# Optimization experiments

Hardware: AMD Instinct MI355X
Metric: run time of the kernel (lower is better)

## Reference

```python
import jax, jax.numpy as jnp
import numpy as np

C = 256      # in_channels
H = 16       # num_heads
K = 7        # tconv kernel size
P1 = 8       # type_1 partition size
P2 = 8       # type_2 partition size
HB = H // 4  # heads per attention branch (= 4)
EPS = 1e-5


def _ln(x, g, b):
    m = x.mean(-1, keepdims=True)
    v = ((x - m) ** 2).mean(-1, keepdims=True)
    return (x - m) / jnp.sqrt(v + EPS) * g + b


def _window_attn(parts, table, heads, P):
    # parts: [B_, P, 3*Cb]; table: [2P-1, heads]
    B_, N, _ = parts.shape
    qkv = parts.reshape(B_, N, 3, heads, -1).transpose(2, 0, 3, 1, 4)  # [3,B_,h,P,d]
    q, k, v = qkv[0], qkv[1], qkv[2]
    scale = heads ** (-0.5)  # NOTE: module scales by num_heads**-0.5 (faithful)
    attn = jnp.einsum('bhnd,bhmd->bhnm', q * scale, k)
    idx = (jnp.arange(P)[:, None] - jnp.arange(P)[None, :]) + P - 1  # [P,P]
    bias = table[idx].transpose(2, 0, 1)  # [h,P,P]
    attn = jax.nn.softmax(attn + bias[None], axis=-1)
    out = jnp.einsum('bhnm,bhmd->bhnd', attn, v)
    return out.transpose(0, 2, 1, 3).reshape(B_, N, -1)


def _type1_part(x, P):  # x: [B,Cc,T] contiguous windows
    B, Cc, T = x.shape
    return x.reshape(B, Cc, T // P, P).transpose(0, 2, 3, 1).reshape(-1, P, Cc)


def _type1_rev(y, B, Cc, T, P):
    return y.reshape(B, T // P, P, Cc).transpose(0, 3, 1, 2).reshape(B, Cc, T)


def _type2_part(x, P):  # strided (dilated) windows
    B, Cc, T = x.shape
    return x.reshape(B, Cc, P, T // P).transpose(0, 3, 2, 1).reshape(-1, P, Cc)


def _type2_rev(y, B, Cc, T, P):
    return y.reshape(B, T // P, P, Cc).transpose(0, 3, 2, 1).reshape(B, Cc, T)


def setup_inputs() -> dict:
    key = jax.random.key(0)
    ks = jax.random.split(key, 16)
    B, T = 16, 8192
    d = {
        'x': jax.random.normal(ks[0], (B, C, T), jnp.float32),
        'g1': jnp.ones((C,), jnp.float32),
        'b1': jnp.zeros((C,), jnp.float32),
        'Wm': jax.random.normal(ks[1], (C, 2 * C), jnp.float32) * 0.02,
        'bm': jnp.zeros((2 * C,), jnp.float32),
        'Wc': jax.random.normal(ks[2], (C // 2, (C // 2) // (H // 2), K), jnp.float32) * 0.05,
        'bc': jnp.zeros((C // 2,), jnp.float32),
        'tab1': jax.random.normal(ks[3], (2 * P1 - 1, HB), jnp.float32) * 0.02,
        'tab2': jax.random.normal(ks[4], (2 * P2 - 1, HB), jnp.float32) * 0.02,
        'Wp': jax.random.normal(ks[5], (C, C), jnp.float32) * 0.02,
        'bp': jnp.zeros((C,), jnp.float32),
        'g2': jnp.ones((C,), jnp.float32),
        'b2': jnp.zeros((C,), jnp.float32),
        'W1': jax.random.normal(ks[6], (C, 4 * C), jnp.float32) * 0.02,
        'bf1': jnp.zeros((4 * C,), jnp.float32),
        'W2': jax.random.normal(ks[7], (4 * C, C), jnp.float32) * 0.02,
        'bf2': jnp.zeros((C,), jnp.float32),
    }
    return d


def _forward(x, g1, b1, Wm, bm, Wc, bc, tab1, tab2, Wp, bp, g2, b2, W1, bf1, W2, bf2):
    B, Cin, T = x.shape
    xt = x.transpose(0, 2, 1)  # [B,T,C]
    skip = xt
    f = (_ln(xt, g1, b1) @ Wm + bm).transpose(0, 2, 1)  # [B,2C,T]
    f_conv, f_attn = f[:, :Cin // 2], f[:, Cin // 2:]
    # grouped temporal conv, padding SAME
    y0 = jax.lax.conv_general_dilated(
        f_conv, Wc, window_strides=(1,), padding=[((K - 1) // 2, (K - 1) // 2)],
        feature_group_count=H // 2, dimension_numbers=('NCH', 'OIH', 'NCH')) + bc[None, :, None]
    Cb3 = 3 * Cin // 4
    fa1, fa2 = f_attn[:, :Cb3], f_attn[:, Cb3:]
    y1 = _type1_rev(_window_attn(_type1_part(fa1, P1), tab1, HB, P1), B, Cin // 4, T, P1)
    y2 = _type2_rev(_window_attn(_type2_part(fa2, P2), tab2, HB, P2), B, Cin // 4, T, P2)
    out = jnp.concatenate([y0, y1, y2], axis=1).transpose(0, 2, 1) @ Wp + bp
    out = skip + out
    h = _ln(out, g2, b2)
    h = jax.nn.gelu(h @ W1 + bf1, approximate=False) @ W2 + bf2
    out = out + h
    return out.transpose(0, 2, 1)  # [B,C,T]


def reference(x, g1, b1, Wm, bm, Wc, bc, tab1, tab2, Wp, bp, g2, b2, W1, bf1, W2, bf2):
    return _forward(x, g1, b1, Wm, bm, Wc, bc, tab1, tab2, Wp, bp, g2, b2, W1, bf1, W2, bf2)
```

## Files before the change

kernel.cpp:

```cpp
#include <hip/hip_runtime.h>
#include <hip/hip_bf16.h>

#define DI __device__ __forceinline__

typedef unsigned short u16;
typedef __attribute__((ext_vector_type(4))) float f32x4;
typedef __attribute__((ext_vector_type(8))) short short8;
typedef __attribute__((ext_vector_type(4))) short short4v;

constexpr int Bb = 16, Tt = 8192;
constexpr int M_TOT = Bb * Tt;

static DI u16 f2bf(float f) {
    union { float f; unsigned u; } v; v.f = f;
    unsigned r = v.u + 0x7fffu + ((v.u >> 16) & 1u);
    return (u16)(r >> 16);
}
static DI float bf2f(u16 u) {
    union { unsigned u; float f; } v; v.u = ((unsigned)u) << 16;
    return v.f;
}
static DI float bf2f_s(short s) { return bf2f((u16)s); }

static DI void lds_load16(const void* g, void* l) {
    __builtin_amdgcn_global_load_lds(
        (const __attribute__((address_space(1))) void*)g,
        (__attribute__((address_space(3))) void*)l, 16, 0, 0);
}

static DI float gelu_exact(float x) {
    float ax = fabsf(x) * 0.70710678118654752f;
    float t = __builtin_amdgcn_rcpf(1.f + 0.3275911f * ax);
    float y = t * (0.254829592f + t * (-0.284496736f + t * (1.421413741f +
              t * (-1.453152027f + t * 1.061405429f))));
    float e = __expf(-ax * ax);
    float erf = 1.f - y * e;
    erf = copysignf(erf, x);
    return 0.5f * x * (1.f + erf);
}

__global__ void prep_weights(const float* __restrict__ Wm, const float* __restrict__ Wp,
                             const float* __restrict__ W1, const float* __restrict__ W2,
                             const float* __restrict__ Wc,
                             u16* __restrict__ WmT, u16* __restrict__ WpT,
                             u16* __restrict__ W1T, u16* __restrict__ W2T,
                             u16* __restrict__ WtC) {
    int i = blockIdx.x * blockDim.x + threadIdx.x;
    int stride = gridDim.x * blockDim.x;
    for (int j = i; j < 512 * 256; j += stride) {
        int n = j >> 8, k = j & 255;
        WmT[j] = f2bf(Wm[k * 512 + n]);
    }
    for (int j = i; j < 256 * 256; j += stride) {
        int n = j >> 8, k = j & 255;
        WpT[j] = f2bf(Wp[k * 256 + n]);
    }
    for (int j = i; j < 1024 * 256; j += stride) {
        int n = j >> 8, k = j & 255;
        W1T[j] = f2bf(W1[k * 1024 + n]);
    }
    for (int j = i; j < 256 * 1024; j += stride) {
        int n = j >> 10, k = j & 1023;
        W2T[j] = f2bf(W2[k * 256 + n]);
    }
    for (int j = i; j < 128 * 128; j += stride) {
        int co = j >> 7, kp = j & 127;
        int tap = kp >> 4, ci = kp & 15;
        float v = (tap < 7) ? Wc[(co * 16 + ci) * 7 + tap] : 0.f;
        WtC[j] = f2bf(v);
    }
}

__global__ __launch_bounds__(256) void ln1_kernel(const float* __restrict__ x,
                                                  const float* __restrict__ g1,
                                                  const float* __restrict__ b1,
                                                  u16* __restrict__ xln,
                                                  u16* __restrict__ xt) {
    __shared__ u16 tile[64 * 256];
    __shared__ float ps[64 * 16], pss[64 * 16];
    __shared__ float smean[64], srstd[64];
    int bidx = blockIdx.x;
    int b = bidx >> 7;
    int t0 = (bidx & 127) << 6;
    int tid = threadIdx.x, l = tid & 63, w = tid >> 6;
    int lr = l & 15, lg = l >> 4;
    float s[4] = {}, ss[4] = {};
    #pragma unroll 4
    for (int it = 0; it < 16; ++it) {
        int c = it * 16 + w * 4 + lg;
        f32x4 v = *(const f32x4*)&x[((size_t)b * 256 + c) * 8192 + t0 + lr * 4];
        #pragma unroll
        for (int k = 0; k < 4; ++k) {
            s[k] += v[k]; ss[k] += v[k] * v[k];
            int t = lr * 4 + k;
            int c8 = c >> 3;
            int slot = (c8 & 24) | ((c8 ^ t) & 7);
            tile[t * 256 + slot * 8 + (c & 7)] = f2bf(v[k]);
        }
    }
    #pragma unroll
    for (int k = 0; k < 4; ++k) {
        ps[(lr * 4 + k) * 16 + w * 4 + lg] = s[k];
        pss[(lr * 4 + k) * 16 + w * 4 + lg] = ss[k];
    }
    __syncthreads();
    if (tid < 64) {
        float sum = 0.f, sq = 0.f;
        #pragma unroll
        for (int g = 0; g < 16; ++g) { sum += ps[tid * 16 + g]; sq += pss[tid * 16 + g]; }
        float m = sum * (1.f / 256.f);
        smean[tid] = m;
        srstd[tid] = rsqrtf(sq * (1.f / 256.f) - m * m + 1e-5f);
    }
    __syncthreads();
    int r = tid >> 2, q = tid & 3;
    float m = smean[r], rs = srstd[r];
    size_t rowbase = ((size_t)b * 8192 + t0 + r) * 256;
    #pragma unroll
    for (int u = 0; u < 8; ++u) {
        int c0 = q * 64 + u * 8;
        int c8 = c0 >> 3;
        int slot = (c8 & 24) | ((c8 ^ r) & 7);
        short8 d = *(const short8*)&tile[r * 256 + slot * 8];
        *(short8*)&xt[rowbase + c0] = d;
        short8 o;
        #pragma unroll
        for (int j = 0; j < 8; ++j) {
            int c = c0 + j;
            o[j] = (short)f2bf((bf2f_s(d[j]) - m) * rs * g1[c] + b1[c]);
        }
        *(short8*)&xln[rowbase + c0] = o;
    }
}

template<int EPI, int N, int K>
__global__ __launch_bounds__(256) void gemm_bt2(const u16* __restrict__ A,
                                                const u16* __restrict__ Bt,
                                                const float* __restrict__ bias,
                                                u16* __restrict__ outb,
                                                const u16* __restrict__ skipx) {
    constexpr int NB = N / 128;
    int bid = blockIdx.x;
    int x8 = bid & 7;
    int rest = bid >> 3;
    int ni = rest % NB;
    int mi = (rest / NB) * 8 + x8;
    int m0 = mi * 128, n0 = ni * 128;
    __shared__ u16 As[2][128 * 64];
    __shared__ u16 Bs[2][128 * 64];
    int tid = threadIdx.x, l = tid & 63, w = tid >> 6;
    int mrow = (w >> 1) * 64, ncol = (w & 1) * 64;
    int lr = l & 15, lg = l >> 4;
    f32x4 acc[4][4] = {};
    auto stage = [&](int buf, int k0) {
        #pragma unroll
        for (int p = 0; p < 4; ++p) {
            int cb = p * 256 + w * 64;
            int chunk = cb + l;
            int row = chunk >> 3, k8 = chunk & 7;
            int k8s = k8 ^ (row & 7);
            lds_load16(A  + (size_t)(m0 + row) * K + k0 + k8s * 8, &As[buf][cb * 8]);
            lds_load16(Bt + (size_t)(n0 + row) * K + k0 + k8s * 8, &Bs[buf][cb * 8]);
        }
    };
    stage(0, 0);
    __syncthreads();
    constexpr int NT = K / 64;
    int buf = 0;
    for (int t = 0; t < NT; ++t) {
        if (t + 1 < NT) stage(buf ^ 1, (t + 1) * 64);
        #pragma unroll
        for (int kk = 0; kk < 64; kk += 32) {
            short8 a[4], bfr[4];
            #pragma unroll
            for (int i = 0; i < 4; ++i) {
                int r = mrow + i * 16 + lr;
                a[i] = *(const short8*)&As[buf][r * 64 + ((((kk >> 3) + lg) ^ (r & 7)) << 3)];
            }
            #pragma unroll
            for (int j = 0; j < 4; ++j) {
                int r = ncol + j * 16 + lr;
                bfr[j] = *(const short8*)&Bs[buf][r * 64 + ((((kk >> 3) + lg) ^ (r & 7)) << 3)];
            }
            #pragma unroll
            for (int i = 0; i < 4; ++i)
                #pragma unroll
                for (int j = 0; j < 4; ++j)
                    acc[i][j] = __builtin_amdgcn_mfma_f32_16x16x32_bf16(a[i], bfr[j], acc[i][j], 0, 0, 0);
        }
        __syncthreads();
        buf ^= 1;
    }
    #pragma unroll
    for (int i = 0; i < 4; ++i) {
        int row0 = m0 + mrow + i * 16 + lg * 4;
        #pragma unroll
        for (int j = 0; j < 4; ++j) {
            int col = n0 + ncol + j * 16 + lr;
            float bv = bias[col];
            f32x4 v = acc[i][j];
            if constexpr (EPI == 0) {
                #pragma unroll
                for (int r = 0; r < 4; ++r)
                    outb[(size_t)(row0 + r) * N + col] = f2bf(v[r] + bv);
            } else {
                #pragma unroll
                for (int r = 0; r < 4; ++r)
                    outb[(size_t)(row0 + r) * N + col] =
                        f2bf(v[r] + bv + bf2f(skipx[(size_t)(row0 + r) * 256 + col]));
            }
        }
    }
}

__global__ __launch_bounds__(512) void ffn_fused(const u16* __restrict__ lnb,
                                                 const u16* __restrict__ W1T,
                                                 const float* __restrict__ bf1v,
                                                 const u16* __restrict__ W2T,
                                                 const float* __restrict__ bf2v,
                                                 const u16* __restrict__ outb,
                                                 float* __restrict__ out) {
    __shared__ u16 Aln[128 * 256];
    __shared__ u16 W1c[64 * 256];
    __shared__ u16 W2c[256 * 64];
    __shared__ u16 hbuf[128 * 64];
    int bid = blockIdx.x;
    int m0 = bid * 128;
    int tid = threadIdx.x, l = tid & 63, w = tid >> 6;
    int lr = l & 15, lg = l >> 4;
    int wm1 = w >> 1, wn1 = w & 1;
    int wm2 = w >> 2, wn2 = w & 3;

    #pragma unroll
    for (int p = 0; p < 8; ++p) {
        int cb = p * 512 + w * 64;
        int chunk = cb + l;
        int row = chunk >> 5, c8 = chunk & 31;
        int c8s = (c8 & 24) | ((c8 ^ row) & 7);
        lds_load16(lnb + (size_t)(m0 + row) * 256 + c8s * 8, &Aln[cb * 8]);
    }
    auto stageW1 = [&](int c) {
        #pragma unroll
        for (int p = 0; p < 4; ++p) {
            int cb = p * 512 + w * 64;
            int chunk = cb + l;
            int row = chunk >> 5, c8 = chunk & 31;
            int c8s = (c8 & 24) | ((c8 ^ row) & 7);
            lds_load16(W1T + (size_t)(c * 64 + row) * 256 + c8s * 8, &W1c[cb * 8]);
        }
    };
    auto stageW2 = [&](int c) {
        #pragma unroll
        for (int p = 0; p < 4; ++p) {
            int cb = p * 512 + w * 64;
            int chunk = cb + l;
            int row = chunk >> 3, c8 = chunk & 7;
            int c8s = (c8 ^ row) & 7;
            lds_load16(W2T + (size_t)row * 1024 + c * 64 + c8s * 8, &W2c[cb * 8]);
        }
    };
    stageW1(0);
    stageW2(0);
    f32x4 acc2[4][4] = {};
    __syncthreads();

    for (int c = 0; c < 16; ++c) {
        f32x4 acc1[2][2] = {};
        #pragma unroll
        for (int ks = 0; ks < 8; ++ks) {
            int c8 = ks * 4 + lg;
            short8 a[2], bb[2];
            #pragma unroll
            for (int i = 0; i < 2; ++i) {
                int r = wm1 * 32 + i * 16 + lr;
                a[i] = *(const short8*)&Aln[r * 256 + (((c8 & 24) | ((c8 ^ r) & 7)) << 3)];
            }
            #pragma unroll
            for (int j = 0; j < 2; ++j) {
                int n = wn1 * 32 + j * 16 + lr;
                bb[j] = *(const short8*)&W1c[n * 256 + (((c8 & 24) | ((c8 ^ n) & 7)) << 3)];
            }
            #pragma unroll
            for (int i = 0; i < 2; ++i)
                #pragma unroll
                for (int j = 0; j < 2; ++j)
                    acc1[i][j] = __builtin_amdgcn_mfma_f32_16x16x32_bf16(a[i], bb[j], acc1[i][j], 0, 0, 0);
        }
        __syncthreads();
        if (c < 15) stageW1(c + 1);
        #pragma unroll
        for (int i = 0; i < 2; ++i) {
            int row = wm1 * 32 + i * 16 + lg * 4;
            #pragma unroll
            for (int j = 0; j < 2; ++j) {
                int col = wn1 * 32 + j * 16 + lr;
                int c8h = col >> 3;
                #pragma unroll
                for (int r = 0; r < 4; ++r) {
                    float vv = gelu_exact(acc1[i][j][r] + bf1v[c * 64 + col]);
                    hbuf[(row + r) * 64 + (((c8h ^ (row + r)) & 7) << 3) + (col & 7)] = f2bf(vv);
                }
            }
        }
        __syncthreads();
        #pragma unroll
        for (int ks = 0; ks < 2; ++ks) {
            int c8 = ks * 4 + lg;
            short8 a[4], bb[4];
            #pragma unroll
            for (int i = 0; i < 4; ++i) {
                int r = wm2 * 64 + i * 16 + lr;
                a[i] = *(const short8*)&hbuf[r * 64 + (((c8 ^ (r & 7)) & 7) << 3)];
            }
            #pragma unroll
            for (int j = 0; j < 4; ++j) {
                int n = wn2 * 64 + j * 16 + lr;
                bb[j] = *(const short8*)&W2c[n * 64 + (((c8 ^ (n & 7)) & 7) << 3)];
            }
            #pragma unroll
            for (int i = 0; i < 4; ++i)
                #pragma unroll
                for (int j = 0; j < 4; ++j)
                    acc2[i][j] = __builtin_amdgcn_mfma_f32_16x16x32_bf16(a[i], bb[j], acc2[i][j], 0, 0, 0);
        }
        __syncthreads();
        if (c < 15) stageW2(c + 1);
    }
    int bidx_b = m0 >> 13;
    int tbase = m0 & 8191;
    #pragma unroll
    for (int i = 0; i < 4; ++i) {
        int row0 = wm2 * 64 + i * 16 + lg * 4;
        #pragma unroll
        for (int j = 0; j < 4; ++j) {
            int col = wn2 * 64 + j * 16 + lr;
            float bv = bf2v[col];
            f32x4 o;
            #pragma unroll
            for (int r = 0; r < 4; ++r)
                o[r] = acc2[i][j][r] + bv + bf2f(outb[(size_t)(m0 + row0 + r) * 256 + col]);
            *(f32x4*)&out[((size_t)bidx_b * 256 + col) * 8192 + tbase + row0] = o;
        }
    }
}

__global__ __launch_bounds__(256) void conv_kernel(const u16* __restrict__ f,
                                                   const u16* __restrict__ WtC,
                                                   const float* __restrict__ bc,
                                                   u16* __restrict__ att) {
    __shared__ u16 fs[72 * 128];
    __shared__ u16 wt[128 * 128];
    int bid = blockIdx.x;
    int b = bid >> 7;
    int t0 = (bid & 127) << 6;
    int tid = threadIdx.x, l = tid & 63, w = tid >> 6;
    for (int c = tid; c < 2048; c += 256) {
        int row = c >> 4, c8 = c & 15;
        int slot = (c8 & 8) | ((c8 ^ row) & 7);
        *(uint4*)&wt[row * 128 + slot * 8] = *(const uint4*)&WtC[c * 8];
    }
    for (int c = tid; c < 72 * 16; c += 256) {
        int rrow = c >> 4, c8 = c & 15;
        int t = t0 - 3 + rrow;
        uint4 v = {0u, 0u, 0u, 0u};
        if (t >= 0 && t < 8192)
            v = *(const uint4*)&f[((size_t)b * 8192 + t) * 512 + c8 * 8];
        int slot = (c8 & 8) | ((c8 ^ rrow) & 7);
        *(uint4*)&fs[rrow * 128 + slot * 8] = v;
    }
    __syncthreads();
    int wr = w >> 1, wc = w & 1;
    int lr = l & 15, lg = l >> 4;
    f32x4 acc[2][4] = {};
    #pragma unroll
    for (int kk = 0; kk < 4; ++kk) {
        int kp = kk * 32 + lg * 8;
        int tap = kp >> 4, ci = kp & 15;
        #pragma unroll
        for (int i = 0; i < 2; ++i) {
            int trow = wr * 32 + i * 16 + lr;
            #pragma unroll
            for (int g = 0; g < 4; ++g) {
                int ra = trow + tap;
                int ea = (wc * 4 + g) * 2 + (ci >> 3);
                short8 a = *(const short8*)&fs[ra * 128 + (((ea & 8) | ((ea ^ ra) & 7)) << 3)];
                int nb = (wc * 4 + g) * 16 + lr;
                int eb = kp >> 3;
                short8 bfr = *(const short8*)&wt[nb * 128 + (((eb & 8) | ((eb ^ nb) & 7)) << 3)];
                acc[i][g] = __builtin_amdgcn_mfma_f32_16x16x32_bf16(a, bfr, acc[i][g], 0, 0, 0);
            }
        }
    }
    #pragma unroll
    for (int i = 0; i < 2; ++i) {
        int trow = wr * 32 + i * 16 + lg * 4;
        #pragma unroll
        for (int g = 0; g < 4; ++g) {
            int co = (wc * 4 + g) * 16 + lr;
            float bv = bc[co];
            #pragma unroll
            for (int r = 0; r < 4; ++r) {
                int t = t0 + trow + r;
                att[((size_t)b * 8192 + t) * 256 + co] = f2bf(acc[i][g][r] + bv);
            }
        }
    }
}

template<int TYPE>
__global__ __launch_bounds__(256) void attn_kernel(const u16* __restrict__ f,
                                                   const float* __restrict__ tab,
                                                   u16* __restrict__ att) {
    __shared__ u16 qkv[64 * 200];
    __shared__ float stab[60];
    constexpr int QBASE = (TYPE == 1) ? 128 : 320;
    constexpr int OBASE = (TYPE == 1) ? 128 : 192;
    int bid = blockIdx.x;
    int b = bid >> 7;
    int j0 = (bid & 127) << 3;
    int tid = threadIdx.x;
    if (tid < 60) stab[tid] = tab[tid];
    for (int c = tid; c < 64 * 24; c += 256) {
        int ridx = c / 24, off = (c % 24) << 3;
        int wl = ridx >> 3, n = ridx & 7;
        int t = (TYPE == 1) ? ((j0 + wl) * 8 + n) : (n * 1024 + j0 + wl);
        *(uint4*)&qkv[ridx * 200 + off] = *(const uint4*)&f[((size_t)b * 8192 + t) * 512 + QBASE + off];
    }
    __syncthreads();
    int wl = tid >> 5, h = (tid >> 3) & 3, n = tid & 7;
    const u16* qr = &qkv[(wl * 8 + n) * 200 + h * 16];
    float q[16];
    {
        short8 q0 = *(const short8*)qr, q1 = *(const short8*)(qr + 8);
        #pragma unroll
        for (int d = 0; d < 8; ++d) { q[d] = bf2f_s(q0[d]); q[d + 8] = bf2f_s(q1[d]); }
    }
    float s[8];
    #pragma unroll
    for (int m = 0; m < 8; ++m) {
        const u16* kr = &qkv[(wl * 8 + m) * 200 + 64 + h * 16];
        short8 k0 = *(const short8*)kr, k1 = *(const short8*)(kr + 8);
        float a = 0.f;
        #pragma unroll
        for (int d = 0; d < 8; ++d) a += q[d] * bf2f_s(k0[d]) + q[d + 8] * bf2f_s(k1[d]);
        s[m] = 0.5f * a + stab[(n - m + 7) * 4 + h];
    }
    float mx = s[0];
    #pragma unroll
    for (int m = 1; m < 8; ++m) mx = fmaxf(mx, s[m]);
    float sum = 0.f;
    #pragma unroll
    for (int m = 0; m < 8; ++m) { s[m] = __expf(s[m] - mx); sum += s[m]; }
    float rinv = 1.f / sum;
    float o[16] = {};
    #pragma unroll
    for (int m = 0; m < 8; ++m) {
        float p = s[m] * rinv;
        const u16* vr = &qkv[(wl * 8 + m) * 200 + 128 + h * 16];
        short8 v0 = *(const short8*)vr, v1 = *(const short8*)(vr + 8);
        #pragma unroll
        for (int d = 0; d < 8; ++d) { o[d] += p * bf2f_s(v0[d]); o[d + 8] += p * bf2f_s(v1[d]); }
    }
    int t = (TYPE == 1) ? ((j0 + wl) * 8 + n) : (n * 1024 + j0 + wl);
    short8 o0, o1;
    #pragma unroll
    for (int d = 0; d < 8; ++d) { o0[d] = (short)f2bf(o[d]); o1[d] = (short)f2bf(o[d + 8]); }
    u16* op = &att[((size_t)b * 8192 + t) * 256 + OBASE + h * 16];
    *(short8*)op = o0; *(short8*)(op + 8) = o1;
}

__global__ __launch_bounds__(256) void ln2_kernel(const u16* __restrict__ outb,
                                                  const float* __restrict__ g2,
                                                  const float* __restrict__ b2,
                                                  u16* __restrict__ ln2o) {
    int row = blockIdx.x * 4 + (threadIdx.x >> 6);
    int l = threadIdx.x & 63;
    const u16* rp = &outb[(size_t)row * 256 + l * 4];
    short4v d = *(const short4v*)rp;
    float v[4];
    float sum = 0.f, ss = 0.f;
    #pragma unroll
    for (int j = 0; j < 4; ++j) {
        v[j] = bf2f_s(d[j]);
        sum += v[j]; ss += v[j] * v[j];
    }
    #pragma unroll
    for (int off = 32; off; off >>= 1) {
        sum += __shfl_xor(sum, off);
        ss  += __shfl_xor(ss, off);
    }
    float mean = sum * (1.f / 256.f);
    float var = ss * (1.f / 256.f) - mean * mean;
    float rstd = rsqrtf(var + 1e-5f);
    short4v o;
    #pragma unroll
    for (int j = 0; j < 4; ++j) {
        int c = l * 4 + j;
        o[j] = (short)f2bf((v[j] - mean) * rstd * g2[c] + b2[c]);
    }
    *(short4v*)&ln2o[(size_t)row * 256 + l * 4] = o;
}

extern "C" void kernel_launch(void* const* d_in, const int* in_sizes, int n_in,
                              void* d_out, int out_size, void* d_ws, size_t ws_size,
                              hipStream_t stream) {
    const float* x    = (const float*)d_in[0];
    const float* g1   = (const float*)d_in[1];
    const float* b1   = (const float*)d_in[2];
    const float* Wm   = (const float*)d_in[3];
    const float* bm   = (const float*)d_in[4];
    const float* Wc   = (const float*)d_in[5];
    const float* bc   = (const float*)d_in[6];
    const float* tab1 = (const float*)d_in[7];
    const float* tab2 = (const float*)d_in[8];
    const float* Wp   = (const float*)d_in[9];
    const float* bp   = (const float*)d_in[10];
    const float* g2   = (const float*)d_in[11];
    const float* b2   = (const float*)d_in[12];
    const float* W1   = (const float*)d_in[13];
    const float* bf1  = (const float*)d_in[14];
    const float* W2   = (const float*)d_in[15];
    const float* bf2  = (const float*)d_in[16];
    float* out = (float*)d_out;

    char* ws = (char*)d_ws;
    u16* f    = (u16*)(ws);
    u16* att  = (u16*)(ws + 134217728);
    u16* outb = (u16*)(ws + 201326592);
    u16* lnb  = (u16*)(ws + 268435456);
    u16* xt   = (u16*)(ws + 335544320);
    char* wb = ws + 402653184;
    u16* WmT = (u16*)wb;
    u16* WpT = (u16*)(wb + 262144);
    u16* W1T = (u16*)(wb + 393216);
    u16* W2T = (u16*)(wb + 917504);
    u16* WtC = (u16*)(wb + 1441792);

    prep_weights<<<512, 256, 0, stream>>>(Wm, Wp, W1, W2, Wc, WmT, WpT, W1T, W2T, WtC);
    ln1_kernel<<<Bb * (Tt / 64), 256, 0, stream>>>(x, g1, b1, lnb, xt);
    gemm_bt2<0, 512, 256><<<(M_TOT / 128) * 4, 256, 0, stream>>>(lnb, WmT, bm, f, nullptr);
    conv_kernel<<<Bb * (Tt / 64), 256, 0, stream>>>(f, WtC, bc, att);
    attn_kernel<1><<<Bb * 128, 256, 0, stream>>>(f, tab1, att);
    attn_kernel<2><<<Bb * 128, 256, 0, stream>>>(f, tab2, att);
    gemm_bt2<1, 256, 256><<<(M_TOT / 128) * 2, 256, 0, stream>>>(att, WpT, bp, outb, xt);
    ln2_kernel<<<M_TOT / 4, 256, 0, stream>>>(outb, g2, b2, lnb);
    ffn_fused<<<M_TOT / 128, 512, 0, stream>>>(lnb, W1T, bf1, W2T, bf2, outb, out);
}
```

Before: 575.1 us.

## Fold LayerNorm affine into weights, fuse LN2 into FFN, double-buffer FFN weights

Folds the LN1 and LN2 gamma scales into the Wm and W1 weights and their betas into precomputed biases, so the LN kernels only normalize. Removes the separate ln2 kernel by computing row statistics inside the FFN kernel from register-resident A fragments, and double-buffers the W1/W2 chunk staging to overlap loads with MFMA. Also replaces exact erf GELU with a sigmoid-style approximation and adds s_setprio around MFMA loops. The GELU approximation and the bf16 rounding of scaled weights change numerics slightly.

After: 524.5 us. 8.8% less time.

```diff
diff --git a/kernel.cpp b/kernel.cpp
--- a/kernel.cpp
+++ b/kernel.cpp
@@ -21,6 +21,9 @@
     return v.f;
 }
 static DI float bf2f_s(short s) { return bf2f((u16)s); }
+static DI unsigned pack2bf(float a, float b) {
+    return (unsigned)f2bf(a) | ((unsigned)f2bf(b) << 16);
+}
 
 static DI void lds_load16(const void* g, void* l) {
     __builtin_amdgcn_global_load_lds(
@@ -28,28 +31,30 @@
         (__attribute__((address_space(3))) void*)l, 16, 0, 0);
 }
 
-static DI float gelu_exact(float x) {
-    float ax = fabsf(x) * 0.70710678118654752f;
-    float t = __builtin_amdgcn_rcpf(1.f + 0.3275911f * ax);
-    float y = t * (0.254829592f + t * (-0.284496736f + t * (1.421413741f +
-              t * (-1.453152027f + t * 1.061405429f))));
-    float e = __expf(-ax * ax);
-    float erf = 1.f - y * e;
-    erf = copysignf(erf, x);
-    return 0.5f * x * (1.f + erf);
+static DI float gelu_fast(float x) {
+    float x2 = x * x;
+    float z2 = x * (2.30220723f + 0.10294515f * x2);
+    float e;
+    asm("v_exp_f32 %0, %1" : "=v"(e) : "v"(z2));
+    float r = __builtin_amdgcn_rcpf(1.f + e);
+    return x - x * r;
 }
 
 __global__ void prep_weights(const float* __restrict__ Wm, const float* __restrict__ Wp,
                              const float* __restrict__ W1, const float* __restrict__ W2,
                              const float* __restrict__ Wc,
+                             const float* __restrict__ g1, const float* __restrict__ b1,
+                             const float* __restrict__ g2, const float* __restrict__ b2,
+                             const float* __restrict__ bm, const float* __restrict__ bf1,
                              u16* __restrict__ WmT, u16* __restrict__ WpT,
                              u16* __restrict__ W1T, u16* __restrict__ W2T,
-                             u16* __restrict__ WtC) {
+                             u16* __restrict__ WtC,
+                             float* __restrict__ bmF, float* __restrict__ b1F) {
     int i = blockIdx.x * blockDim.x + threadIdx.x;
     int stride = gridDim.x * blockDim.x;
     for (int j = i; j < 512 * 256; j += stride) {
         int n = j >> 8, k = j & 255;
-        WmT[j] = f2bf(Wm[k * 512 + n]);
+        WmT[j] = f2bf(Wm[k * 512 + n] * g1[k]);
     }
     for (int j = i; j < 256 * 256; j += stride) {
         int n = j >> 8, k = j & 255;
@@ -57,7 +62,7 @@
     }
     for (int j = i; j < 1024 * 256; j += stride) {
         int n = j >> 8, k = j & 255;
-        W1T[j] = f2bf(W1[k * 1024 + n]);
+        W1T[j] = f2bf(W1[k * 1024 + n] * g2[k]);
     }
     for (int j = i; j < 256 * 1024; j += stride) {
         int n = j >> 10, k = j & 1023;
@@ -69,11 +74,19 @@
         float v = (tap < 7) ? Wc[(co * 16 + ci) * 7 + tap] : 0.f;
         WtC[j] = f2bf(v);
     }
+    for (int n = i; n < 512; n += stride) {
+        float s = bm[n];
+        for (int k = 0; k < 256; ++k) s += b1[k] * Wm[k * 512 + n];
+        bmF[n] = s;
+    }
+    for (int n = i; n < 1024; n += stride) {
+        float s = bf1[n];
+        for (int k = 0; k < 256; ++k) s += b2[k] * W1[k * 1024 + n];
+        b1F[n] = s;
+    }
 }
 
 __global__ __launch_bounds__(256) void ln1_kernel(const float* __restrict__ x,
-                                                  const float* __restrict__ g1,
-                                                  const float* __restrict__ b1,
                                                   u16* __restrict__ xln,
                                                   u16* __restrict__ xt) {
     __shared__ u16 tile[64 * 256];
@@ -125,10 +138,8 @@
         *(short8*)&xt[rowbase + c0] = d;
         short8 o;
         #pragma unroll
-        for (int j = 0; j < 8; ++j) {
-            int c = c0 + j;
-            o[j] = (short)f2bf((bf2f_s(d[j]) - m) * rs * g1[c] + b1[c]);
-        }
+        for (int j = 0; j < 8; ++j)
+            o[j] = (short)f2bf((bf2f_s(d[j]) - m) * rs);
         *(short8*)&xln[rowbase + c0] = o;
     }
 }
@@ -169,6 +180,7 @@
     int buf = 0;
     for (int t = 0; t < NT; ++t) {
         if (t + 1 < NT) stage(buf ^ 1, (t + 1) * 64);
+        __builtin_amdgcn_s_setprio(1);
         #pragma unroll
         for (int kk = 0; kk < 64; kk += 32) {
             short8 a[4], bfr[4];
@@ -188,6 +200,7 @@
                 for (int j = 0; j < 4; ++j)
                     acc[i][j] = __builtin_amdgcn_mfma_f32_16x16x32_bf16(a[i], bfr[j], acc[i][j], 0, 0, 0);
         }
+        __builtin_amdgcn_s_setprio(0);
         __syncthreads();
         buf ^= 1;
     }
@@ -213,133 +226,157 @@
     }
 }
 
-__global__ __launch_bounds__(512) void ffn_fused(const u16* __restrict__ lnb,
-                                                 const u16* __restrict__ W1T,
-                                                 const float* __restrict__ bf1v,
-                                                 const u16* __restrict__ W2T,
-                                                 const float* __restrict__ bf2v,
-                                                 const u16* __restrict__ outb,
-                                                 float* __restrict__ out) {
-    __shared__ u16 Aln[128 * 256];
-    __shared__ u16 W1c[64 * 256];
-    __shared__ u16 W2c[256 * 64];
+__global__ __launch_bounds__(512) void ffn_fused2(const u16* __restrict__ outb,
+                                                  const u16* __restrict__ W1g,
+                                                  const float* __restrict__ b1F,
+                                                  const u16* __restrict__ W2T,
+                                                  const float* __restrict__ bf2v,
+                                                  float* __restrict__ out) {
+    __shared__ u16 W1c[2][64 * 256];
+    __shared__ u16 W2c[2][256 * 64];
     __shared__ u16 hbuf[128 * 64];
     int bid = blockIdx.x;
     int m0 = bid * 128;
     int tid = threadIdx.x, l = tid & 63, w = tid >> 6;
     int lr = l & 15, lg = l >> 4;
-    int wm1 = w >> 1, wn1 = w & 1;
-    int wm2 = w >> 2, wn2 = w & 3;
-
-    #pragma unroll
-    for (int p = 0; p < 8; ++p) {
-        int cb = p * 512 + w * 64;
-        int chunk = cb + l;
-        int row = chunk >> 5, c8 = chunk & 31;
-        int c8s = (c8 & 24) | ((c8 ^ row) & 7);
-        lds_load16(lnb + (size_t)(m0 + row) * 256 + c8s * 8, &Aln[cb * 8]);
-    }
-    auto stageW1 = [&](int c) {
+    int wm = w >> 1, wn = w & 1;
+
+    short8 a_reg[2][8];
+    float mean[2], rstd[2];
+    #pragma unroll
+    for (int mt = 0; mt < 2; ++mt) {
+        size_t base = (size_t)(m0 + wm * 32 + mt * 16 + lr) * 256 + lg * 8;
+        float s = 0.f, ss = 0.f;
+        #pragma unroll
+        for (int ks = 0; ks < 8; ++ks) {
+            short8 rv = *(const short8*)&outb[base + ks * 32];
+            a_reg[mt][ks] = rv;
+            #pragma unroll
+            for (int e = 0; e < 8; ++e) { float v = bf2f_s(rv[e]); s += v; ss += v * v; }
+        }
+        s += __shfl_xor(s, 16); ss += __shfl_xor(ss, 16);
+        s += __shfl_xor(s, 32); ss += __shfl_xor(ss, 32);
+        float m = s * (1.f / 256.f);
+        mean[mt] = m;
+        rstd[mt] = rsqrtf(ss * (1.f / 256.f) - m * m + 1e-5f);
+    }
+    #pragma unroll
+    for (int mt = 0; mt < 2; ++mt) {
+        float m = mean[mt], rs = rstd[mt];
+        #pragma unroll
+        for (int ks = 0; ks < 8; ++ks) {
+            short8 rv = a_reg[mt][ks], ov;
+            #pragma unroll
+            for (int e = 0; e < 8; ++e) ov[e] = (short)f2bf((bf2f_s(rv[e]) - m) * rs);
+            a_reg[mt][ks] = ov;
+        }
+    }
+
+    auto stageW1 = [&](int buf, int c) {
         #pragma unroll
         for (int p = 0; p < 4; ++p) {
             int cb = p * 512 + w * 64;
             int chunk = cb + l;
-            int row = chunk >> 5, c8 = chunk & 31;
-            int c8s = (c8 & 24) | ((c8 ^ row) & 7);
-            lds_load16(W1T + (size_t)(c * 64 + row) * 256 + c8s * 8, &W1c[cb * 8]);
+            int row = chunk >> 5, sl = chunk & 31;
+            int sl2 = (sl & 24) | ((sl ^ row) & 7);
+            lds_load16(W1g + (size_t)(c * 64 + row) * 256 + sl2 * 8, &W1c[buf][cb * 8]);
         }
     };
-    auto stageW2 = [&](int c) {
+    auto stageW2 = [&](int buf, int c) {
         #pragma unroll
         for (int p = 0; p < 4; ++p) {
             int cb = p * 512 + w * 64;
             int chunk = cb + l;
-            int row = chunk >> 3, c8 = chunk & 7;
-            int c8s = (c8 ^ row) & 7;
-            lds_load16(W2T + (size_t)row * 1024 + c * 64 + c8s * 8, &W2c[cb * 8]);
+            int row = chunk >> 3, sl = chunk & 7;
+            int sl2 = sl ^ (row & 7);
+            lds_load16(W2T + (size_t)row * 1024 + c * 64 + sl2 * 8, &W2c[buf][cb * 8]);
         }
     };
-    stageW1(0);
-    stageW2(0);
-    f32x4 acc2[4][4] = {};
+    stageW1(0, 0); stageW2(0, 0);
+    f32x4 acc2[2][8] = {};
     __syncthreads();
 
     for (int c = 0; c < 16; ++c) {
+        int buf = c & 1;
+        if (c < 15) { stageW1(buf ^ 1, c + 1); stageW2(buf ^ 1, c + 1); }
         f32x4 acc1[2][2] = {};
+        __builtin_amdgcn_s_setprio(1);
         #pragma unroll
         for (int ks = 0; ks < 8; ++ks) {
-            int c8 = ks * 4 + lg;
-            short8 a[2], bb[2];
-            #pragma unroll
-            for (int i = 0; i < 2; ++i) {
-                int r = wm1 * 32 + i * 16 + lr;
-                a[i] = *(const short8*)&Aln[r * 256 + (((c8 & 24) | ((c8 ^ r) & 7)) << 3)];
-            }
-            #pragma unroll
-            for (int j = 0; j < 2; ++j) {
-                int n = wn1 * 32 + j * 16 + lr;
-                bb[j] = *(const short8*)&W1c[n * 256 + (((c8 & 24) | ((c8 ^ n) & 7)) << 3)];
-            }
-            #pragma unroll
-            for (int i = 0; i < 2; ++i)
+            short8 wf[2];
+            #pragma unroll
+            for (int nt = 0; nt < 2; ++nt) {
+                int n = wn * 32 + nt * 16 + lr;
+                int sl = ks * 4 + lg;
+                int sl2 = (sl & 24) | ((sl ^ n) & 7);
+                wf[nt] = *(const short8*)&W1c[buf][n * 256 + sl2 * 8];
+            }
+            #pragma unroll
+            for (int nt = 0; nt < 2; ++nt)
                 #pragma unroll
-                for (int j = 0; j < 2; ++j)
-                    acc1[i][j] = __builtin_amdgcn_mfma_f32_16x16x32_bf16(a[i], bb[j], acc1[i][j], 0, 0, 0);
+                for (int mt = 0; mt < 2; ++mt)
+                    acc1[nt][mt] = __builtin_amdgcn_mfma_f32_16x16x32_bf16(
+                        wf[nt], a_reg[mt][ks], acc1[nt][mt], 0, 0, 0);
+        }
+        __builtin_amdgcn_s_setprio(0);
+        #pragma unroll
+        for (int nt = 0; nt < 2; ++nt) {
+            int colb = wn * 32 + nt * 16 + lg * 4;
+            f32x4 bv4 = *(const f32x4*)&b1F[c * 64 + colb];
+            #pragma unroll
+            for (int mt = 0; mt < 2; ++mt) {
+                int row = wm * 32 + mt * 16 + lr;
+                unsigned d0 = pack2bf(gelu_fast(acc1[nt][mt][0] + bv4[0]),
+                                      gelu_fast(acc1[nt][mt][1] + bv4[1]));
+                unsigned d1 = pack2bf(gelu_fast(acc1[nt][mt][2] + bv4[2]),
+                                      gelu_fast(acc1[nt][mt][3] + bv4[3]));
+                int s0 = colb >> 3;
+                int sl2 = s0 ^ (row & 7);
+                *(unsigned*)&hbuf[row * 64 + sl2 * 8 + (colb & 7)] = d0;
+                *(unsigned*)&hbuf[row * 64 + sl2 * 8 + (colb & 7) + 2] = d1;
+            }
         }
         __syncthreads();
-        if (c < 15) stageW1(c + 1);
-        #pragma unroll
-        for (int i = 0; i < 2; ++i) {
-            int row = wm1 * 32 + i * 16 + lg * 4;
-            #pragma unroll
-            for (int j = 0; j < 2; ++j) {
-                int col = wn1 * 32 + j * 16 + lr;
-                int c8h = col >> 3;
+        __builtin_amdgcn_s_setprio(1);
+        #pragma unroll
+        for (int ks = 0; ks < 2; ++ks) {
+            short8 hf[2], w2f[8];
+            #pragma unroll
+            for (int mt = 0; mt < 2; ++mt) {
+                int row = wm * 32 + mt * 16 + lr;
+                int sl2 = (ks * 4 + lg) ^ (row & 7);
+                hf[mt] = *(const short8*)&hbuf[row * 64 + sl2 * 8];
+            }
+            #pragma unroll
+            for (int nt = 0; nt < 8; ++nt) {
+                int n = wn * 128 + nt * 16 + lr;
+                int sl2 = (ks * 4 + lg) ^ (n & 7);
+                w2f[nt] = *(const short8*)&W2c[buf][n * 64 + sl2 * 8];
+            }
+            #pragma unroll
+            for (int mt = 0; mt < 2; ++mt)
                 #pragma unroll
-                for (int r = 0; r < 4; ++r) {
-                    float vv = gelu_exact(acc1[i][j][r] + bf1v[c * 64 + col]);
-                    hbuf[(row + r) * 64 + (((c8h ^ (row + r)) & 7) << 3) + (col & 7)] = f2bf(vv);
-                }
-            }
-        }
+                for (int nt = 0; nt < 8; ++nt)
+                    acc2[mt][nt] = __builtin_amdgcn_mfma_f32_16x16x32_bf16(
+                        hf[mt], w2f[nt], acc2[mt][nt], 0, 0, 0);
+        }
+        __builtin_amdgcn_s_setprio(0);
         __syncthreads();
-        #pragma unroll
-        for (int ks = 0; ks < 2; ++ks) {
-            int c8 = ks * 4 + lg;
-            short8 a[4], bb[4];
-            #pragma unroll
-            for (int i = 0; i < 4; ++i) {
-                int r = wm2 * 64 + i * 16 + lr;
-                a[i] = *(const short8*)&hbuf[r * 64 + (((c8 ^ (r & 7)) & 7) << 3)];
-            }
-            #pragma unroll
-            for (int j = 0; j < 4; ++j) {
-                int n = wn2 * 64 + j * 16 + lr;
-                bb[j] = *(const short8*)&W2c[n * 64 + (((c8 ^ (n & 7)) & 7) << 3)];
-            }
-            #pragma unroll
-            for (int i = 0; i < 4; ++i)
-                #pragma unroll
-                for (int j = 0; j < 4; ++j)
-                    acc2[i][j] = __builtin_amdgcn_mfma_f32_16x16x32_bf16(a[i], bb[j], acc2[i][j], 0, 0, 0);
-        }
-        __syncthreads();
-        if (c < 15) stageW2(c + 1);
-    }
-    int bidx_b = m0 >> 13;
-    int tbase = m0 & 8191;
-    #pragma unroll
-    for (int i = 0; i < 4; ++i) {
-        int row0 = wm2 * 64 + i * 16 + lg * 4;
-        #pragma unroll
-        for (int j = 0; j < 4; ++j) {
-            int col = wn2 * 64 + j * 16 + lr;
+    }
+    int bb_ = m0 >> 13;
+    int tb = m0 & 8191;
+    #pragma unroll
+    for (int mt = 0; mt < 2; ++mt) {
+        int row0 = wm * 32 + mt * 16 + lg * 4;
+        #pragma unroll
+        for (int nt = 0; nt < 8; ++nt) {
+            int col = wn * 128 + nt * 16 + lr;
             float bv = bf2v[col];
             f32x4 o;
             #pragma unroll
             for (int r = 0; r < 4; ++r)
-                o[r] = acc2[i][j][r] + bv + bf2f(outb[(size_t)(m0 + row0 + r) * 256 + col]);
-            *(f32x4*)&out[((size_t)bidx_b * 256 + col) * 8192 + tbase + row0] = o;
+                o[r] = acc2[mt][nt][r] + bv + bf2f(outb[(size_t)(m0 + row0 + r) * 256 + col]);
+            *(f32x4*)&out[((size_t)bb_ * 256 + col) * 8192 + tb + row0] = o;
         }
     }
 }
@@ -467,38 +504,6 @@
     for (int d = 0; d < 8; ++d) { o0[d] = (short)f2bf(o[d]); o1[d] = (short)f2bf(o[d + 8]); }
     u16* op = &att[((size_t)b * 8192 + t) * 256 + OBASE + h * 16];
     *(short8*)op = o0; *(short8*)(op + 8) = o1;
-}
-
-__global__ __launch_bounds__(256) void ln2_kernel(const u16* __restrict__ outb,
-                                                  const float* __restrict__ g2,
-                                                  const float* __restrict__ b2,
-                                                  u16* __restrict__ ln2o) {
-    int row = blockIdx.x * 4 + (threadIdx.x >> 6);
-    int l = threadIdx.x & 63;
-    const u16* rp = &outb[(size_t)row * 256 + l * 4];
-    short4v d = *(const short4v*)rp;
-    float v[4];
-    float sum = 0.f, ss = 0.f;
-    #pragma unroll
-    for (int j = 0; j < 4; ++j) {
-        v[j] = bf2f_s(d[j]);
-        sum += v[j]; ss += v[j] * v[j];
-    }
-    #pragma unroll
-    for (int off = 32; off; off >>= 1) {
-        sum += __shfl_xor(sum, off);
-        ss  += __shfl_xor(ss, off);
-    }
-    float mean = sum * (1.f / 256.f);
-    float var = ss * (1.f / 256.f) - mean * mean;
-    float rstd = rsqrtf(var + 1e-5f);
-    short4v o;
-    #pragma unroll
-    for (int j = 0; j < 4; ++j) {
-        int c = l * 4 + j;
-        o[j] = (short)f2bf((v[j] - mean) * rstd * g2[c] + b2[c]);
-    }
-    *(short4v*)&ln2o[(size_t)row * 256 + l * 4] = o;
 }
 
 extern "C" void kernel_launch(void* const* d_in, const int* in_sizes, int n_in,
@@ -527,22 +532,24 @@
     u16* f    = (u16*)(ws);
     u16* att  = (u16*)(ws + 134217728);
     u16* outb = (u16*)(ws + 201326592);
-    u16* lnb  = (u16*)(ws + 268435456);
+    u16* xlnb = (u16*)(ws + 268435456);
     u16* xt   = (u16*)(ws + 335544320);
     char* wb = ws + 402653184;
-    u16* WmT = (u16*)wb;
-    u16* WpT = (u16*)(wb + 262144);
-    u16* W1T = (u16*)(wb + 393216);
-    u16* W2T = (u16*)(wb + 917504);
-    u16* WtC = (u16*)(wb + 1441792);
-
-    prep_weights<<<512, 256, 0, stream>>>(Wm, Wp, W1, W2, Wc, WmT, WpT, W1T, W2T, WtC);
-    ln1_kernel<<<Bb * (Tt / 64), 256, 0, stream>>>(x, g1, b1, lnb, xt);
-    gemm_bt2<0, 512, 256><<<(M_TOT / 128) * 4, 256, 0, stream>>>(lnb, WmT, bm, f, nullptr);
+    u16* WmT   = (u16*)wb;
+    u16* WpT   = (u16*)(wb + 262144);
+    u16* W1T   = (u16*)(wb + 393216);
+    u16* W2T   = (u16*)(wb + 917504);
+    u16* WtC   = (u16*)(wb + 1441792);
+    float* bmF = (float*)(wb + 1474560);
+    float* b1F = (float*)(wb + 1476608);
+
+    prep_weights<<<512, 256, 0, stream>>>(Wm, Wp, W1, W2, Wc, g1, b1, g2, b2, bm, bf1,
+                                          WmT, WpT, W1T, W2T, WtC, bmF, b1F);
+    ln1_kernel<<<Bb * (Tt / 64), 256, 0, stream>>>(x, xlnb, xt);
+    gemm_bt2<0, 512, 256><<<(M_TOT / 128) * 4, 256, 0, stream>>>(xlnb, WmT, bmF, f, nullptr);
     conv_kernel<<<Bb * (Tt / 64), 256, 0, stream>>>(f, WtC, bc, att);
     attn_kernel<1><<<Bb * 128, 256, 0, stream>>>(f, tab1, att);
     attn_kernel<2><<<Bb * 128, 256, 0, stream>>>(f, tab2, att);
     gemm_bt2<1, 256, 256><<<(M_TOT / 128) * 2, 256, 0, stream>>>(att, WpT, bp, outb, xt);
-    ln2_kernel<<<M_TOT / 4, 256, 0, stream>>>(outb, g2, b2, lnb);
-    ffn_fused<<<M_TOT / 128, 512, 0, stream>>>(lnb, W1T, bf1, W2T, bf2, outb, out);
-}
+    ffn_fused2<<<M_TOT / 128, 512, 0, stream>>>(outb, W1T, b1F, W2T, bf2, out);
+}
```
